# Optimization experiments

Hardware: AMD Instinct MI355X
Metric: run time of the kernel (lower is better)

Reference implementation:

```python
import jax, jax.numpy as jnp
import numpy as np


def setup_inputs() -> dict:
    key = jax.random.key(0)
    k1, k2 = jax.random.split(key)
    B, D, T = 16, 256, 2048
    L, K = 8, 1024
    x = jax.random.normal(k1, (B, D, T), dtype=jnp.float32)
    codebooks = jax.random.normal(k2, (L, K, D), dtype=jnp.float32)
    return {"x": x, "codebooks": codebooks}


def reference(x, codebooks):
    """Residual vector quantization (SoundStream-style).

    x:         (B, D, T) latent features
    codebooks: (L, K, D) one codebook per residual layer

    Returns:
        output:  (B, D, T) sum of selected embeddings across layers
        indices: (B, L, T) selected codebook indices per layer
    """
    r0 = jnp.transpose(x, (0, 2, 1))  # (B, T, D)

    def step(carry, W):
        residual, acc = carry
        # squared euclidean distance: ||r||^2 - 2 r.W^T + ||w||^2  -> (B, T, K)
        dots = jnp.einsum("btd,kd->btk", residual, W)
        dist = (
            jnp.sum(residual * residual, axis=-1, keepdims=True)
            - 2.0 * dots
            + jnp.sum(W * W, axis=-1)
        )
        idx = jnp.argmin(dist, axis=-1)          # (B, T)
        q = W[idx]                               # (B, T, D) gather
        return (residual - q, acc + q), idx

    (_, quantized), indices = jax.lax.scan(
        step, (r0, jnp.zeros_like(r0)), codebooks
    )
    output = jnp.transpose(quantized, (0, 2, 1))        # (B, D, T)
    indices = jnp.transpose(indices, (1, 0, 2))          # (B, L, T)
    return output, indices
```

## Files before the change

### kernel.cpp

```cpp
#include <hip/hip_runtime.h>

#define D_ 256
#define T_ 2048
#define K_ 1024
#define L_ 8
#define B_ 16
#define THETA 0.5f
#define ECT 40
#define NTILE 64

typedef _Float16 f16x8 __attribute__((ext_vector_type(8)));
typedef float    f32x4 __attribute__((ext_vector_type(4)));

typedef const __attribute__((address_space(1))) unsigned int* gas1_t;
typedef __attribute__((address_space(3))) unsigned int*       las3_t;

__device__ __forceinline__ void gls16(const void* g, void* l) {
    __builtin_amdgcn_global_load_lds((gas1_t)g, (las3_t)l, 16, 0, 0);
}
__device__ __forceinline__ void gls4(const void* g, void* l) {
    __builtin_amdgcn_global_load_lds((gas1_t)g, (las3_t)l, 4, 0, 0);
}

__device__ __forceinline__ unsigned long long packkey(float sc, unsigned cand) {
    const unsigned fb = __float_as_uint(sc);
    const unsigned ob = fb ^ ((unsigned)((int)fb >> 31) | 0x80000000u);
    return (((unsigned long long)ob) << 32) | cand;
}
__device__ __forceinline__ float unpackf(unsigned long long key) {
    const unsigned ob = (unsigned)(key >> 32);
    const unsigned fb = (ob & 0x80000000u) ? (ob ^ 0x80000000u) : ~ob;
    return __uint_as_float(fb);
}
__device__ __forceinline__ unsigned short f2h_bits(float s) {
    union { _Float16 f; unsigned short u; } cv; cv.f = (_Float16)s; return cv.u;
}
__device__ __forceinline__ float h_bits2f(unsigned short u) {
    union { _Float16 f; unsigned short u; } cv; cv.u = u; return (float)cv.f;
}

__global__ __launch_bounds__(256, 4)
void rvq_ww_kernel(const float* __restrict__ cb, float* __restrict__ ww) {
    const int row  = blockIdx.x * 4 + (threadIdx.x >> 6);
    const int lane = threadIdx.x & 63;
    const float4 v = *reinterpret_cast<const float4*>(cb + (size_t)row * D_ + (lane << 2));
    float s = v.x * v.x + v.y * v.y + v.z * v.z + v.w * v.w;
    #pragma unroll
    for (int off = 1; off < 64; off <<= 1) s += __shfl_xor(s, off, 64);
    if (lane == 0) ww[row] = s;
}

__global__ __launch_bounds__(256)
void rvq_cvtp_kernel(const float* __restrict__ cb, _Float16* __restrict__ cbp) {
    const int e    = blockIdx.x * 256 + threadIdx.x;
    const int gt   = e >> 12, q = e & 4095;
    const int lane = q & 63, nk = q >> 6;
    const int n = nk & 7, kk = nk >> 3, c4 = lane & 15, g = lane >> 4;
    const int l = gt >> 3, ch = gt & 7;
    const float* src = cb + (size_t)(l * 1024 + ch * 128 + n * 16 + c4) * D_ + kk * 32 + g * 8;
    const float4 a = *reinterpret_cast<const float4*>(src);
    const float4 b = *reinterpret_cast<const float4*>(src + 4);
    f16x8 v;
    v[0] = (_Float16)a.x; v[1] = (_Float16)a.y; v[2] = (_Float16)a.z; v[3] = (_Float16)a.w;
    v[4] = (_Float16)b.x; v[5] = (_Float16)b.y; v[6] = (_Float16)b.z; v[7] = (_Float16)b.w;
    *reinterpret_cast<f16x8*>(cbp + (size_t)e * 8) = v;
}

__global__ __launch_bounds__(512, 2)
void rvq_main_kernel(const float* __restrict__ x, const float* __restrict__ cbf,
                     const _Float16* __restrict__ cb16p, const float* __restrict__ ww,
                     float* __restrict__ out) {
    __shared__ __align__(16) _Float16 bstage[2][32768];
    __shared__ float    wwlds[2][128];
    __shared__ unsigned elist[8][16][ECT];
    __shared__ int      ecnt[8][16];

    const int tid  = threadIdx.x;
    const int lane = tid & 63;
    const int wv   = tid >> 6;
    const int c4   = lane & 15;
    const int g    = lane >> 4;
    const int tg   = blockIdx.x * 128 + wv * 16 + c4;
    const int b    = tg >> 11;
    const int tl   = tg & (T_ - 1);
    const size_t xbase = ((size_t)b << 19) + tl;

    auto stage_tile = [&](int gt) {
        const _Float16* s = cb16p + ((size_t)gt * 4096 + wv * 512 + lane) * 8;
        char* d = (char*)bstage[gt & 1] + wv * 8192;
        #pragma unroll
        for (int i = 0; i < 8; ++i)
            gls16(s + i * 512, d + i * 1024);
        if (wv < 2)
            gls4(ww + gt * 128 + wv * 64 + lane, &wwlds[gt & 1][wv * 64]);
    };

    stage_tile(0);

    float r_[64];
    #pragma unroll
    for (int kk = 0; kk < 8; ++kk)
        #pragma unroll
        for (int e = 0; e < 8; ++e)
            r_[kk * 8 + e] = x[xbase + (size_t)(kk * 32 + g * 8 + e) * T_];

    __syncthreads();

    #pragma unroll 1
    for (int l = 0; l < L_; ++l) {
        const float* __restrict__ cblf = cbf + (size_t)l * K_ * D_;
        const float* __restrict__ wwl  = ww + l * K_;

        if (lane < 16) ecnt[wv][lane] = 0;

        float rrv;
        {
            float Tk[8];
            #pragma unroll
            for (int kk = 0; kk < 8; ++kk) {
                float4 v;
                v.x = r_[kk * 8 + 0]; v.y = r_[kk * 8 + 1];
                v.z = r_[kk * 8 + 2]; v.w = r_[kk * 8 + 3];
                float s = v.x * v.x + v.y * v.y + v.z * v.z + v.w * v.w;
                float4 u;
                u.x = r_[kk * 8 + 4]; u.y = r_[kk * 8 + 5];
                u.z = r_[kk * 8 + 6]; u.w = r_[kk * 8 + 7];
                float s2 = u.x * u.x + u.y * u.y + u.z * u.z + u.w * u.w;
                const float p  = s + s2;
                const float po = __shfl_xor(p, 16, 64);
                const float q  = p + po;
                const float qo = __shfl_xor(q, 32, 64);
                Tk[kk] = q + qo;
            }
            const float u01 = Tk[0] + Tk[1], u23 = Tk[2] + Tk[3];
            const float u45 = Tk[4] + Tk[5], u67 = Tk[6] + Tk[7];
            rrv = (u01 + u23) + (u45 + u67);
        }

        float    bsc[4], bth[4];
        unsigned bcd[4];
        #pragma unroll
        for (int j = 0; j < 4; ++j) {
            bsc[j] = __builtin_inff(); bth[j] = __builtin_inff(); bcd[j] = 0u;
        }

        #pragma unroll 1
        for (int c = 0; c < 8; ++c) {
            const int gt = l * 8 + c;
            if (gt + 1 < NTILE) stage_tile(gt + 1);

            const _Float16* bufp = bstage[gt & 1];
            const float*    wwp  = wwlds[gt & 1];
            const int base = c * 128;

            #pragma unroll
            for (int np = 0; np < 4; ++np) {
                const int n0 = np * 2, n1 = np * 2 + 1;
                f32x4 a0 = (f32x4){0.f, 0.f, 0.f, 0.f};
                f32x4 a1 = (f32x4){0.f, 0.f, 0.f, 0.f};
                #pragma unroll
                for (int kk = 0; kk < 8; ++kk) {
                    f16x8 fx;
                    #pragma unroll
                    for (int e = 0; e < 8; ++e) fx[e] = (_Float16)r_[kk * 8 + e];
                    const f16x8 b0 = *reinterpret_cast<const f16x8*>(
                        bufp + ((kk * 8 + n0) * 64 + lane) * 8);
                    const f16x8 b1 = *reinterpret_cast<const f16x8*>(
                        bufp + ((kk * 8 + n1) * 64 + lane) * 8);
                    a0 = __builtin_amdgcn_mfma_f32_16x16x32_f16(fx, b0, a0, 0, 0, 0);
                    a1 = __builtin_amdgcn_mfma_f32_16x16x32_f16(fx, b1, a1, 0, 0, 0);
                }
                #pragma unroll
                for (int n2 = 0; n2 < 2; ++n2) {
                    const f32x4 av = n2 ? a1 : a0;
                    const unsigned cand = (unsigned)(base + (np * 2 + n2) * 16 + c4);
                    const float wwv = wwp[(np * 2 + n2) * 16 + c4];
                    #pragma unroll
                    for (int j = 0; j < 4; ++j) {
                        const float sc = fmaf(-2.0f, av[j], wwv);
                        const int tj = g * 4 + j;
                        if (sc < bsc[j]) {
                            if (bsc[j] <= sc + THETA) {
                                const int p = atomicAdd(&ecnt[wv][tj], 1);
                                if (p < ECT)
                                    elist[wv][tj][p] = (bcd[j] << 16) | f2h_bits(bsc[j]);
                            }
                            bsc[j] = sc; bcd[j] = cand; bth[j] = sc + THETA;
                        } else if (sc <= bth[j]) {
                            const int p = atomicAdd(&ecnt[wv][tj], 1);
                            if (p < ECT)
                                elist[wv][tj][p] = (cand << 16) | f2h_bits(sc);
                        }
                    }
                }
            }

            __syncthreads();
        }

        unsigned long long bkl[4];
        #pragma unroll
        for (int j = 0; j < 4; ++j) bkl[j] = packkey(bsc[j], bcd[j]);

        unsigned long long gk[4];
        #pragma unroll
        for (int j = 0; j < 4; ++j) {
            unsigned long long k0 = bkl[j];
            #pragma unroll
            for (int off = 1; off < 16; off <<= 1) {
                const unsigned long long k2 = __shfl_xor(k0, off, 64);
                if (k2 < k0) k0 = k2;
            }
            gk[j] = k0;
            if (bkl[j] != k0) {
                const float ls = unpackf(bkl[j]);
                if (ls <= unpackf(k0) + THETA) {
                    const int tj = g * 4 + j;
                    const int p = atomicAdd(&ecnt[wv][tj], 1);
                    if (p < ECT)
                        elist[wv][tj][p] =
                            (((unsigned)(bkl[j] & 0xffffull)) << 16) | f2h_bits(ls);
                }
            }
        }

        unsigned bc0 = (unsigned)(gk[0] & 0xffffffffull);
        unsigned bc1 = (unsigned)(gk[1] & 0xffffffffull);
        unsigned bc2 = (unsigned)(gk[2] & 0xffffffffull);
        unsigned bc3 = (unsigned)(gk[3] & 0xffffffffull);
        float gm0 = unpackf(gk[0]), gm1 = unpackf(gk[1]);
        float gm2 = unpackf(gk[2]), gm3 = unpackf(gk[3]);
        const int srcl = (c4 >> 2) << 4;
        const unsigned w0 = __shfl(bc0, srcl, 64);
        const unsigned w1 = __shfl(bc1, srcl, 64);
        const unsigned w2 = __shfl(bc2, srcl, 64);
        const unsigned w3 = __shfl(bc3, srcl, 64);
        const float s0 = __shfl(gm0, srcl, 64);
        const float s1 = __shfl(gm1, srcl, 64);
        const float s2 = __shfl(gm2, srcl, 64);
        const float s3 = __shfl(gm3, srcl, 64);
        const unsigned wa = (c4 & 1) ? w1 : w0;
        const unsigned wb = (c4 & 1) ? w3 : w2;
        const unsigned wincand = (c4 & 2) ? wb : wa;
        const float sa = (c4 & 1) ? s1 : s0;
        const float sb = (c4 & 1) ? s3 : s2;
        const float gminmy = (c4 & 2) ? sb : sa;

        unsigned long long bestk;
        {
            const float* wp = cblf + (size_t)wincand * D_;
            float4 wA = *reinterpret_cast<const float4*>(wp + g * 8);
            float4 wB = *reinterpret_cast<const float4*>(wp + g * 8 + 4);
            float4 nA = *reinterpret_cast<const float4*>(wp + 32 + g * 8);
            float4 nB = *reinterpret_cast<const float4*>(wp + 32 + g * 8 + 4);
            float a0 = 0.0f;
            #pragma unroll
            for (int s = 0; s < 32; ++s) {
                const int kk = s >> 2;
                if ((s & 3) == g) {
                    a0 = fmaf(wA.x, r_[kk * 8 + 0], a0);
                    a0 = fmaf(wA.y, r_[kk * 8 + 1], a0);
                    a0 = fmaf(wA.z, r_[kk * 8 + 2], a0);
                    a0 = fmaf(wA.w, r_[kk * 8 + 3], a0);
                    a0 = fmaf(wB.x, r_[kk * 8 + 4], a0);
                    a0 = fmaf(wB.y, r_[kk * 8 + 5], a0);
                    a0 = fmaf(wB.z, r_[kk * 8 + 6], a0);
                    a0 = fmaf(wB.w, r_[kk * 8 + 7], a0);
                    wA = nA; wB = nB;
                    if (kk + 2 < 8) {
                        nA = *reinterpret_cast<const float4*>(wp + (kk + 2) * 32 + g * 8);
                        nB = *reinterpret_cast<const float4*>(wp + (kk + 2) * 32 + g * 8 + 4);
                    }
                }
                a0 = __shfl(a0, (lane + 48) & 63, 64);
            }
            a0 = __shfl(a0, c4, 64);
            const float scw = __fadd_rn(__fsub_rn(rrv, __fmul_rn(2.0f, a0)), wwl[wincand]);
            bestk = packkey(scw, wincand);
        }

        {
            const int myn = min(ecnt[wv][c4], ECT);
            const float gth = gminmy + THETA + 0.5f;
            #pragma unroll 1
            for (int i = 0; i < myn; ++i) {
                const unsigned e  = elist[wv][c4][i];
                const unsigned ec = e >> 16;
                const float hsc = h_bits2f((unsigned short)(e & 0xffffu));
                if (ec == wincand || hsc > gth) continue;
                const float* ep = cblf + (size_t)ec * D_;
                float4 wA = *reinterpret_cast<const float4*>(ep + g * 8);
                float4 wB = *reinterpret_cast<const float4*>(ep + g * 8 + 4);
                float4 nA = *reinterpret_cast<const float4*>(ep + 32 + g * 8);
                float4 nB = *reinterpret_cast<const float4*>(ep + 32 + g * 8 + 4);
                float q = 0.0f;
                #pragma unroll
                for (int s = 0; s < 32; ++s) {
                    const int kk = s >> 2;
                    if ((s & 3) == g) {
                        q = fmaf(wA.x, r_[kk * 8 + 0], q);
                        q = fmaf(wA.y, r_[kk * 8 + 1], q);
                        q = fmaf(wA.z, r_[kk * 8 + 2], q);
                        q = fmaf(wA.w, r_[kk * 8 + 3], q);
                        q = fmaf(wB.x, r_[kk * 8 + 4], q);
                        q = fmaf(wB.y, r_[kk * 8 + 5], q);
                        q = fmaf(wB.z, r_[kk * 8 + 6], q);
                        q = fmaf(wB.w, r_[kk * 8 + 7], q);
                        wA = nA; wB = nB;
                        if (kk + 2 < 8) {
                            nA = *reinterpret_cast<const float4*>(ep + (kk + 2) * 32 + g * 8);
                            nB = *reinterpret_cast<const float4*>(ep + (kk + 2) * 32 + g * 8 + 4);
                        }
                    }
                    q = __shfl(q, (lane + 48) & 63, 64);
                }
                q = __shfl(q, c4, 64);
                const float sce = __fadd_rn(__fsub_rn(rrv, __fmul_rn(2.0f, q)), wwl[ec]);
                const unsigned long long k2 = packkey(sce, ec);
                if (k2 < bestk) bestk = k2;
            }
        }

        const unsigned fc = (unsigned)(bestk & 0xffffffffull);
        if (g == 0)
            out[(size_t)B_ * D_ * T_ + ((size_t)b * L_ + l) * T_ + tl] = (float)fc;

        {
            const float* up = cblf + (size_t)fc * D_;
            #pragma unroll
            for (int kk = 0; kk < 8; ++kk) {
                const float4 ua = *reinterpret_cast<const float4*>(up + kk * 32 + g * 8);
                const float4 ub = *reinterpret_cast<const float4*>(up + kk * 32 + g * 8 + 4);
                r_[kk * 8 + 0] = __fsub_rn(r_[kk * 8 + 0], ua.x);
                r_[kk * 8 + 1] = __fsub_rn(r_[kk * 8 + 1], ua.y);
                r_[kk * 8 + 2] = __fsub_rn(r_[kk * 8 + 2], ua.z);
                r_[kk * 8 + 3] = __fsub_rn(r_[kk * 8 + 3], ua.w);
                r_[kk * 8 + 4] = __fsub_rn(r_[kk * 8 + 4], ub.x);
                r_[kk * 8 + 5] = __fsub_rn(r_[kk * 8 + 5], ub.y);
                r_[kk * 8 + 6] = __fsub_rn(r_[kk * 8 + 6], ub.z);
                r_[kk * 8 + 7] = __fsub_rn(r_[kk * 8 + 7], ub.w);
            }
        }
    }

    #pragma unroll
    for (int kk = 0; kk < 8; ++kk)
        #pragma unroll
        for (int e = 0; e < 8; ++e) {
            const size_t gi = xbase + (size_t)(kk * 32 + g * 8 + e) * T_;
            out[gi] = __fsub_rn(x[gi], r_[kk * 8 + e]);
        }
}

extern "C" void kernel_launch(void* const* d_in, const int* in_sizes, int n_in,
                              void* d_out, int out_size, void* d_ws, size_t ws_size,
                              hipStream_t stream) {
    const float* x  = (const float*)d_in[0];
    const float* cb = (const float*)d_in[1];
    float* out = (float*)d_out;
    float*    ww    = (float*)d_ws;
    _Float16* cb16p = (_Float16*)((char*)d_ws + 32768);

    hipLaunchKernelGGL(rvq_ww_kernel,   dim3((L_ * K_) / 4), dim3(256), 0, stream, cb, ww);
    hipLaunchKernelGGL(rvq_cvtp_kernel, dim3(1024), dim3(256), 0, stream, cb, cb16p);
    hipLaunchKernelGGL(rvq_main_kernel, dim3((B_ * T_) / 128), dim3(512), 0, stream,
                       x, cb, cb16p, ww, out);
}
```

Before: 462.6 us.

## Parallelize exact rescoring per token via LDS residual and atomicMin

The exact fp32 rescoring of the winner and near-tie candidates now runs with four threads per token. Each thread walks the full residual from shared memory, read from a pool that aliases the staging buffer, and the results merge through a 64-bit atomicMin. Before, each candidate was scored serially with a 4-way split and 32 shuffle steps. The prefetch of the next layer's first tile moves to after rescoring because the pool is reused, and extra __syncthreads are added. This trades the cross-layer prefetch overlap and added barriers for less serial shuffle-heavy rescoring work.

```diff
diff --git a/kernel.cpp b/kernel.cpp
--- a/kernel.cpp
+++ b/kernel.cpp
@@ -7,7 +7,6 @@
 #define B_ 16
 #define THETA 0.5f
 #define ECT 40
-#define NTILE 64
 
 typedef _Float16 f16x8 __attribute__((ext_vector_type(8)));
 typedef float    f32x4 __attribute__((ext_vector_type(4)));
@@ -70,10 +69,12 @@
 void rvq_main_kernel(const float* __restrict__ x, const float* __restrict__ cbf,
                      const _Float16* __restrict__ cb16p, const float* __restrict__ ww,
                      float* __restrict__ out) {
-    __shared__ __align__(16) _Float16 bstage[2][32768];
-    __shared__ float    wwlds[2][128];
-    __shared__ unsigned elist[8][16][ECT];
-    __shared__ int      ecnt[8][16];
+    __shared__ __align__(16) char pool[133120];
+    __shared__ unsigned           elist[8][16][ECT];
+    __shared__ int                ecnt[8][16];
+    __shared__ float              rrs[128];
+    __shared__ unsigned long long fin64[128];
+    __shared__ unsigned long long ex64[128];
 
     const int tid  = threadIdx.x;
     const int lane = tid & 63;
@@ -87,12 +88,13 @@
 
     auto stage_tile = [&](int gt) {
         const _Float16* s = cb16p + ((size_t)gt * 4096 + wv * 512 + lane) * 8;
-        char* d = (char*)bstage[gt & 1] + wv * 8192;
+        char* d = pool + (gt & 1) * 65536 + wv * 8192;
         #pragma unroll
         for (int i = 0; i < 8; ++i)
             gls16(s + i * 512, d + i * 1024);
         if (wv < 2)
-            gls4(ww + gt * 128 + wv * 64 + lane, &wwlds[gt & 1][wv * 64]);
+            gls4(ww + gt * 128 + wv * 64 + lane,
+                 pool + 131072 + ((gt & 1) * 128 + wv * 64 + lane - lane) * 4);
     };
 
     stage_tile(0);
@@ -147,10 +149,10 @@
         #pragma unroll 1
         for (int c = 0; c < 8; ++c) {
             const int gt = l * 8 + c;
-            if (gt + 1 < NTILE) stage_tile(gt + 1);
-
-            const _Float16* bufp = bstage[gt & 1];
-            const float*    wwp  = wwlds[gt & 1];
+            if (c < 7) stage_tile(gt + 1);
+
+            const _Float16* bufp = (const _Float16*)(pool + (gt & 1) * 65536);
+            const float*    wwp  = (const float*)(pool + 131072) + (gt & 1) * 128;
             const int base = c * 128;
 
             #pragma unroll
@@ -198,130 +200,114 @@
             __syncthreads();
         }
 
-        unsigned long long bkl[4];
-        #pragma unroll
-        for (int j = 0; j < 4; ++j) bkl[j] = packkey(bsc[j], bcd[j]);
-
-        unsigned long long gk[4];
-        #pragma unroll
-        for (int j = 0; j < 4; ++j) {
-            unsigned long long k0 = bkl[j];
-            #pragma unroll
-            for (int off = 1; off < 16; off <<= 1) {
-                const unsigned long long k2 = __shfl_xor(k0, off, 64);
-                if (k2 < k0) k0 = k2;
-            }
-            gk[j] = k0;
-            if (bkl[j] != k0) {
-                const float ls = unpackf(bkl[j]);
-                if (ls <= unpackf(k0) + THETA) {
-                    const int tj = g * 4 + j;
-                    const int p = atomicAdd(&ecnt[wv][tj], 1);
-                    if (p < ECT)
-                        elist[wv][tj][p] =
-                            (((unsigned)(bkl[j] & 0xffffull)) << 16) | f2h_bits(ls);
-                }
-            }
-        }
-
-        unsigned bc0 = (unsigned)(gk[0] & 0xffffffffull);
-        unsigned bc1 = (unsigned)(gk[1] & 0xffffffffull);
-        unsigned bc2 = (unsigned)(gk[2] & 0xffffffffull);
-        unsigned bc3 = (unsigned)(gk[3] & 0xffffffffull);
-        float gm0 = unpackf(gk[0]), gm1 = unpackf(gk[1]);
-        float gm2 = unpackf(gk[2]), gm3 = unpackf(gk[3]);
-        const int srcl = (c4 >> 2) << 4;
-        const unsigned w0 = __shfl(bc0, srcl, 64);
-        const unsigned w1 = __shfl(bc1, srcl, 64);
-        const unsigned w2 = __shfl(bc2, srcl, 64);
-        const unsigned w3 = __shfl(bc3, srcl, 64);
-        const float s0 = __shfl(gm0, srcl, 64);
-        const float s1 = __shfl(gm1, srcl, 64);
-        const float s2 = __shfl(gm2, srcl, 64);
-        const float s3 = __shfl(gm3, srcl, 64);
-        const unsigned wa = (c4 & 1) ? w1 : w0;
-        const unsigned wb = (c4 & 1) ? w3 : w2;
-        const unsigned wincand = (c4 & 2) ? wb : wa;
-        const float sa = (c4 & 1) ? s1 : s0;
-        const float sb = (c4 & 1) ? s3 : s2;
-        const float gminmy = (c4 & 2) ? sb : sa;
-
-        unsigned long long bestk;
-        {
-            const float* wp = cblf + (size_t)wincand * D_;
-            float4 wA = *reinterpret_cast<const float4*>(wp + g * 8);
-            float4 wB = *reinterpret_cast<const float4*>(wp + g * 8 + 4);
-            float4 nA = *reinterpret_cast<const float4*>(wp + 32 + g * 8);
-            float4 nB = *reinterpret_cast<const float4*>(wp + 32 + g * 8 + 4);
-            float a0 = 0.0f;
-            #pragma unroll
-            for (int s = 0; s < 32; ++s) {
-                const int kk = s >> 2;
-                if ((s & 3) == g) {
-                    a0 = fmaf(wA.x, r_[kk * 8 + 0], a0);
-                    a0 = fmaf(wA.y, r_[kk * 8 + 1], a0);
-                    a0 = fmaf(wA.z, r_[kk * 8 + 2], a0);
-                    a0 = fmaf(wA.w, r_[kk * 8 + 3], a0);
-                    a0 = fmaf(wB.x, r_[kk * 8 + 4], a0);
-                    a0 = fmaf(wB.y, r_[kk * 8 + 5], a0);
-                    a0 = fmaf(wB.z, r_[kk * 8 + 6], a0);
-                    a0 = fmaf(wB.w, r_[kk * 8 + 7], a0);
-                    wA = nA; wB = nB;
-                    if (kk + 2 < 8) {
-                        nA = *reinterpret_cast<const float4*>(wp + (kk + 2) * 32 + g * 8);
-                        nB = *reinterpret_cast<const float4*>(wp + (kk + 2) * 32 + g * 8 + 4);
+        {
+            float* rp = (float*)pool + (wv * 16 + c4) * 260 + g * 8;
+            #pragma unroll
+            for (int kk = 0; kk < 8; ++kk) {
+                float4 v0; v0.x = r_[kk*8+0]; v0.y = r_[kk*8+1]; v0.z = r_[kk*8+2]; v0.w = r_[kk*8+3];
+                float4 v1; v1.x = r_[kk*8+4]; v1.y = r_[kk*8+5]; v1.z = r_[kk*8+6]; v1.w = r_[kk*8+7];
+                *reinterpret_cast<float4*>(rp + kk * 32)     = v0;
+                *reinterpret_cast<float4*>(rp + kk * 32 + 4) = v1;
+            }
+        }
+        if (g == 0) rrs[wv * 16 + c4] = rrv;
+        if (tid < 128) ex64[tid] = ~0ull;
+
+        {
+            unsigned long long bkl[4];
+            #pragma unroll
+            for (int j = 0; j < 4; ++j) bkl[j] = packkey(bsc[j], bcd[j]);
+            #pragma unroll
+            for (int j = 0; j < 4; ++j) {
+                unsigned long long k0 = bkl[j];
+                #pragma unroll
+                for (int off = 1; off < 16; off <<= 1) {
+                    const unsigned long long k2 = __shfl_xor(k0, off, 64);
+                    if (k2 < k0) k0 = k2;
+                }
+                if (bkl[j] != k0) {
+                    const float ls = unpackf(bkl[j]);
+                    if (ls <= unpackf(k0) + THETA) {
+                        const int tj = g * 4 + j;
+                        const int p = atomicAdd(&ecnt[wv][tj], 1);
+                        if (p < ECT)
+                            elist[wv][tj][p] =
+                                (((unsigned)(bkl[j] & 0xffffull)) << 16) | f2h_bits(ls);
                     }
                 }
-                a0 = __shfl(a0, (lane + 48) & 63, 64);
-            }
-            a0 = __shfl(a0, c4, 64);
-            const float scw = __fadd_rn(__fsub_rn(rrv, __fmul_rn(2.0f, a0)), wwl[wincand]);
-            bestk = packkey(scw, wincand);
-        }
-
-        {
-            const int myn = min(ecnt[wv][c4], ECT);
-            const float gth = gminmy + THETA + 0.5f;
+                if (c4 == 0) fin64[wv * 16 + g * 4 + j] = k0;
+            }
+        }
+        __syncthreads();
+
+        {
+            const int tok = tid >> 2, sub = tid & 3;
+            const int twv = tok >> 4, ttj = tok & 15;
+            const unsigned long long fk = fin64[tok];
+            const unsigned wincand = (unsigned)(fk & 0xffffffffull);
+            const float rrt = rrs[tok];
+            const float gth = unpackf(fk) + THETA + 0.5f;
+            const float* rp = (const float*)pool + tok * 260;
+            unsigned long long bk = ~0ull;
+
+            if (sub == 0) {
+                const float* wp = cblf + (size_t)wincand * D_;
+                float a0 = 0.0f;
+                #pragma unroll 4
+                for (int dc = 0; dc < D_; dc += 8) {
+                    const float4 ra = *reinterpret_cast<const float4*>(rp + dc);
+                    const float4 rb = *reinterpret_cast<const float4*>(rp + dc + 4);
+                    const float4 wa4 = *reinterpret_cast<const float4*>(wp + dc);
+                    const float4 wb4 = *reinterpret_cast<const float4*>(wp + dc + 4);
+                    a0 = fmaf(wa4.x, ra.x, a0);
+                    a0 = fmaf(wa4.y, ra.y, a0);
+                    a0 = fmaf(wa4.z, ra.z, a0);
+                    a0 = fmaf(wa4.w, ra.w, a0);
+                    a0 = fmaf(wb4.x, rb.x, a0);
+                    a0 = fmaf(wb4.y, rb.y, a0);
+                    a0 = fmaf(wb4.z, rb.z, a0);
+                    a0 = fmaf(wb4.w, rb.w, a0);
+                }
+                const float scw = __fadd_rn(__fsub_rn(rrt, __fmul_rn(2.0f, a0)), wwl[wincand]);
+                bk = packkey(scw, wincand);
+            }
+
+            const int myn = min(ecnt[twv][ttj], ECT);
             #pragma unroll 1
-            for (int i = 0; i < myn; ++i) {
-                const unsigned e  = elist[wv][c4][i];
+            for (int i = sub; i < myn; i += 4) {
+                const unsigned e  = elist[twv][ttj][i];
                 const unsigned ec = e >> 16;
                 const float hsc = h_bits2f((unsigned short)(e & 0xffffu));
                 if (ec == wincand || hsc > gth) continue;
                 const float* ep = cblf + (size_t)ec * D_;
-                float4 wA = *reinterpret_cast<const float4*>(ep + g * 8);
-                float4 wB = *reinterpret_cast<const float4*>(ep + g * 8 + 4);
-                float4 nA = *reinterpret_cast<const float4*>(ep + 32 + g * 8);
-                float4 nB = *reinterpret_cast<const float4*>(ep + 32 + g * 8 + 4);
                 float q = 0.0f;
-                #pragma unroll
-                for (int s = 0; s < 32; ++s) {
-                    const int kk = s >> 2;
-                    if ((s & 3) == g) {
-                        q = fmaf(wA.x, r_[kk * 8 + 0], q);
-                        q = fmaf(wA.y, r_[kk * 8 + 1], q);
-                        q = fmaf(wA.z, r_[kk * 8 + 2], q);
-                        q = fmaf(wA.w, r_[kk * 8 + 3], q);
-                        q = fmaf(wB.x, r_[kk * 8 + 4], q);
-                        q = fmaf(wB.y, r_[kk * 8 + 5], q);
-                        q = fmaf(wB.z, r_[kk * 8 + 6], q);
-                        q = fmaf(wB.w, r_[kk * 8 + 7], q);
-                        wA = nA; wB = nB;
-                        if (kk + 2 < 8) {
-                            nA = *reinterpret_cast<const float4*>(ep + (kk + 2) * 32 + g * 8);
-                            nB = *reinterpret_cast<const float4*>(ep + (kk + 2) * 32 + g * 8 + 4);
-                        }
-                    }
-                    q = __shfl(q, (lane + 48) & 63, 64);
-                }
-                q = __shfl(q, c4, 64);
-                const float sce = __fadd_rn(__fsub_rn(rrv, __fmul_rn(2.0f, q)), wwl[ec]);
+                #pragma unroll 4
+                for (int dc = 0; dc < D_; dc += 8) {
+                    const float4 ra = *reinterpret_cast<const float4*>(rp + dc);
+                    const float4 rb = *reinterpret_cast<const float4*>(rp + dc + 4);
+                    const float4 wa4 = *reinterpret_cast<const float4*>(ep + dc);
+                    const float4 wb4 = *reinterpret_cast<const float4*>(ep + dc + 4);
+                    q = fmaf(wa4.x, ra.x, q);
+                    q = fmaf(wa4.y, ra.y, q);
+                    q = fmaf(wa4.z, ra.z, q);
+                    q = fmaf(wa4.w, ra.w, q);
+                    q = fmaf(wb4.x, rb.x, q);
+                    q = fmaf(wb4.y, rb.y, q);
+                    q = fmaf(wb4.z, rb.z, q);
+                    q = fmaf(wb4.w, rb.w, q);
+                }
+                const float sce = __fadd_rn(__fsub_rn(rrt, __fmul_rn(2.0f, q)), wwl[ec]);
                 const unsigned long long k2 = packkey(sce, ec);
-                if (k2 < bestk) bestk = k2;
-            }
-        }
-
-        const unsigned fc = (unsigned)(bestk & 0xffffffffull);
+                if (k2 < bk) bk = k2;
+            }
+
+            if (bk != ~0ull) atomicMin(&ex64[tok], bk);
+        }
+        __syncthreads();
+
+        if (l + 1 < L_) stage_tile((l + 1) * 8);
+
+        const unsigned fc = (unsigned)(ex64[wv * 16 + c4] & 0xffffffffull);
         if (g == 0)
             out[(size_t)B_ * D_ * T_ + ((size_t)b * L_ + l) * T_ + tl] = (float)fc;
 
@@ -341,6 +327,7 @@
                 r_[kk * 8 + 7] = __fsub_rn(r_[kk * 8 + 7], ub.w);
             }
         }
+        __syncthreads();
     }
 
     #pragma unroll
```

After: 453.6 us. Within noise of the previous version (-2.0%).
